# Kernel optimization log

Measured on AMD Instinct MI355X. Metric: run time of the kernel, lower is better.

## Reference

```python
import jax, jax.numpy as jnp
import numpy as np

N_HEAD = 16

def setup_inputs() -> dict:
    key = jax.random.key(0)
    ks = jax.random.split(key, 5)
    B, T, D = 2, 2048, 1024
    BN = 1024  # bottleneck_dim
    s = 0.02
    return {
        "x": jax.random.normal(ks[0], (B, T, D), dtype=jnp.float32),
        "w_qkv": jax.random.normal(ks[1], (3 * BN, D), dtype=jnp.float32) * s,
        "b_qkv": jax.random.normal(ks[2], (3 * BN,), dtype=jnp.float32) * s,
        "w_proj": jax.random.normal(ks[3], (D, BN), dtype=jnp.float32) * s,
        "b_proj": jax.random.normal(ks[4], (D,), dtype=jnp.float32) * s,
        "top_k": 64,
    }

def reference(x, w_qkv, b_qkv, w_proj, b_proj, top_k):
    B, T, D = x.shape
    H = N_HEAD
    BN = w_qkv.shape[0] // 3
    Dh = BN // H
    # qkv projection; torch Linear: y = x @ W^T + b
    qkv = (x @ w_qkv.T + b_qkv).reshape(B, T, 3, H, Dh)
    q = jnp.moveaxis(qkv[:, :, 0], 1, 2)  # (B,H,T,Dh)
    k = jnp.moveaxis(qkv[:, :, 1], 1, 2)
    v = jnp.moveaxis(qkv[:, :, 2], 1, 2)
    att = jnp.einsum('bhqd,bhkd->bhqk', q, k) * (1.0 / np.sqrt(Dh).astype(np.float32))
    # SparseK mask: keep only top-k scores per query row, mask rest before softmax
    topv = jax.lax.top_k(att, top_k)[0]          # (B,H,T,top_k)
    thresh = topv[..., -1:]                      # kth largest per row
    att = jnp.where(att >= thresh, att, -jnp.inf)
    att = jax.nn.softmax(att, axis=-1)
    y = jnp.einsum('bhqk,bhkd->bhqd', att, v)    # (B,H,T,Dh)
    y = y.transpose(0, 2, 1, 3).reshape(B, T, BN)
    return y @ w_proj.T + b_proj
```

## Files before the change

### kernel.cpp

```cpp
#include <hip/hip_runtime.h>
#include <hip/hip_bf16.h>
#include <math.h>

#define Bz 2
#define Tz 2048
#define Dz 1024
#define Hz 16
#define DHz 64
#define BNz 1024
#define TOPKz 64
#define QBLK 16
#define CAND_MAX 176
#define BAND 8e-5f
#define SLO  -20.0f
#define SBINW 0.15625f
#define SBINR 6.4f
#define LDSB 40
#define HSTR 257

typedef __attribute__((ext_vector_type(8))) short bf16x8;
typedef __attribute__((ext_vector_type(4))) short s16x4;
typedef __attribute__((ext_vector_type(4))) float f32x4;

__device__ __forceinline__ short f2bf(float f) {
  unsigned u = __float_as_uint(f);
  return (short)((u + 0x7FFFu + ((u >> 16) & 1u)) >> 16);
}
__device__ __forceinline__ float bf2f(short b) {
  return __uint_as_float(((unsigned)(unsigned short)b) << 16);
}
__device__ __forceinline__ unsigned f2s(float f) {
  unsigned u = __float_as_uint(f);
  return (u & 0x80000000u) ? ~u : (u | 0x80000000u);
}
__device__ __forceinline__ float s2f(unsigned u) {
  return __uint_as_float((u & 0x80000000u) ? (u & 0x7FFFFFFFu) : ~u);
}

__global__ __launch_bounds__(256) void qkv_gemm_split(
    const float* __restrict__ A, const float* __restrict__ W,
    const float* __restrict__ bias,
    float* __restrict__ q32, float* __restrict__ k32,
    short* __restrict__ kbf, float* __restrict__ v32)
{
  __shared__ __align__(16) short Ah[128][LDSB];
  __shared__ __align__(16) short Am[128][LDSB];
  __shared__ __align__(16) short Al[128][LDSB];
  __shared__ __align__(16) short Bh[64][LDSB];
  __shared__ __align__(16) short Bm[64][LDSB];
  __shared__ __align__(16) short Bl[64][LDSB];

  const int tid = threadIdx.x;
  const int lane = tid & 63, wid = tid >> 6;
  const int m0 = blockIdx.y * 128, n0 = blockIdx.x * 64;
  const int bcol = lane & 15, lgrp = lane >> 4;

  f32x4 acch[2][4], accl[2][4];
#pragma unroll
  for (int ms = 0; ms < 2; ++ms)
#pragma unroll
    for (int nt = 0; nt < 4; ++nt) {
      acch[ms][nt] = (f32x4){0.f, 0.f, 0.f, 0.f};
      accl[ms][nt] = (f32x4){0.f, 0.f, 0.f, 0.f};
    }

  const int arow = tid >> 1, ak = (tid & 1) * 16;
  const int brow = tid >> 2, bk = (tid & 3) * 8;
  const float* Ald = A + (size_t)(m0 + arow) * Dz + ak;
  const float* Wld = W + (size_t)(n0 + brow) * Dz + bk;

  for (int kt = 0; kt < Dz; kt += 32) {
    float4 a4[4], b4[2];
#pragma unroll
    for (int j = 0; j < 4; ++j) a4[j] = *(const float4*)(Ald + kt + 4*j);
#pragma unroll
    for (int j = 0; j < 2; ++j) b4[j] = *(const float4*)(Wld + kt + 4*j);
    __syncthreads();

#pragma unroll
    for (int j = 0; j < 4; ++j) {
      float vv[4] = {a4[j].x, a4[j].y, a4[j].z, a4[j].w};
      s16x4 h4, m4, l4;
#pragma unroll
      for (int e = 0; e < 4; ++e) {
        short hh = f2bf(vv[e]);
        float r1 = vv[e] - bf2f(hh);
        short mm = f2bf(r1);
        float r2 = r1 - bf2f(mm);
        h4[e] = hh; m4[e] = mm; l4[e] = f2bf(r2);
      }
      *(s16x4*)&Ah[arow][ak + 4*j] = h4;
      *(s16x4*)&Am[arow][ak + 4*j] = m4;
      *(s16x4*)&Al[arow][ak + 4*j] = l4;
    }
#pragma unroll
    for (int j = 0; j < 2; ++j) {
      float vv[4] = {b4[j].x, b4[j].y, b4[j].z, b4[j].w};
      s16x4 h4, m4, l4;
#pragma unroll
      for (int e = 0; e < 4; ++e) {
        short hh = f2bf(vv[e]);
        float r1 = vv[e] - bf2f(hh);
        short mm = f2bf(r1);
        float r2 = r1 - bf2f(mm);
        h4[e] = hh; m4[e] = mm; l4[e] = f2bf(r2);
      }
      *(s16x4*)&Bh[brow][bk + 4*j] = h4;
      *(s16x4*)&Bm[brow][bk + 4*j] = m4;
      *(s16x4*)&Bl[brow][bk + 4*j] = l4;
    }
    __syncthreads();

    bf16x8 ah[2], am[2], al[2];
#pragma unroll
    for (int ms = 0; ms < 2; ++ms) {
      int rr = wid*32 + ms*16 + bcol;
      ah[ms] = *(const bf16x8*)&Ah[rr][lgrp*8];
      am[ms] = *(const bf16x8*)&Am[rr][lgrp*8];
      al[ms] = *(const bf16x8*)&Al[rr][lgrp*8];
    }
#pragma unroll
    for (int nt = 0; nt < 4; ++nt) {
      int nr = nt*16 + bcol;
      bf16x8 bh = *(const bf16x8*)&Bh[nr][lgrp*8];
      bf16x8 bm = *(const bf16x8*)&Bm[nr][lgrp*8];
      bf16x8 bl = *(const bf16x8*)&Bl[nr][lgrp*8];
#pragma unroll
      for (int ms = 0; ms < 2; ++ms) {
        acch[ms][nt] = __builtin_amdgcn_mfma_f32_16x16x32_bf16(ah[ms], bh, acch[ms][nt], 0, 0, 0);
        accl[ms][nt] = __builtin_amdgcn_mfma_f32_16x16x32_bf16(ah[ms], bm, accl[ms][nt], 0, 0, 0);
        accl[ms][nt] = __builtin_amdgcn_mfma_f32_16x16x32_bf16(am[ms], bh, accl[ms][nt], 0, 0, 0);
        accl[ms][nt] = __builtin_amdgcn_mfma_f32_16x16x32_bf16(am[ms], bm, accl[ms][nt], 0, 0, 0);
        accl[ms][nt] = __builtin_amdgcn_mfma_f32_16x16x32_bf16(ah[ms], bl, accl[ms][nt], 0, 0, 0);
        accl[ms][nt] = __builtin_amdgcn_mfma_f32_16x16x32_bf16(al[ms], bh, accl[ms][nt], 0, 0, 0);
      }
    }
  }

#pragma unroll
  for (int ms = 0; ms < 2; ++ms)
#pragma unroll
    for (int nt = 0; nt < 4; ++nt)
#pragma unroll
      for (int rv = 0; rv < 4; ++rv) {
        int m = m0 + wid*32 + ms*16 + lgrp*4 + rv;
        int n = n0 + nt*16 + bcol;
        double val = (double)acch[ms][nt][rv] + (double)accl[ms][nt][rv] + (double)bias[n];
        int bb = m >> 11;
        int t = m & 2047;
        if (n < BNz) {
          int h = n >> 6, d = n & 63;
          q32[(((size_t)(bb*Hz + h))*Tz + t)*DHz + d] = (float)val;
        } else if (n < 2*BNz) {
          int h = (n - BNz) >> 6, d = n & 63;
          size_t bh = (size_t)(bb*Hz + h);
          float vf = (float)val;
          k32[(bh*Tz + t)*DHz + d] = vf;
          kbf[(bh*Tz + t)*DHz + d] = f2bf(vf);
        } else {
          int h = (n - 2*BNz) >> 6, d = n & 63;
          v32[(((size_t)(bb*Hz + h))*Tz + t)*DHz + d] = (float)val;
        }
      }
}

__global__ __launch_bounds__(256) void proj_gemm_split(
    const float* __restrict__ A, const float* __restrict__ W,
    const float* __restrict__ bias, float* __restrict__ out)
{
  __shared__ __align__(16) short Ah[128][LDSB];
  __shared__ __align__(16) short Am[128][LDSB];
  __shared__ __align__(16) short Al[128][LDSB];
  __shared__ __align__(16) short Bh[64][LDSB];
  __shared__ __align__(16) short Bm[64][LDSB];
  __shared__ __align__(16) short Bl[64][LDSB];

  const int tid = threadIdx.x;
  const int lane = tid & 63, wid = tid >> 6;
  const int m0 = blockIdx.y * 128, n0 = blockIdx.x * 64;
  const int bcol = lane & 15, lgrp = lane >> 4;

  f32x4 acch[2][4], accl[2][4];
#pragma unroll
  for (int ms = 0; ms < 2; ++ms)
#pragma unroll
    for (int nt = 0; nt < 4; ++nt) {
      acch[ms][nt] = (f32x4){0.f, 0.f, 0.f, 0.f};
      accl[ms][nt] = (f32x4){0.f, 0.f, 0.f, 0.f};
    }

  const int arow = tid >> 1, ak = (tid & 1) * 16;
  const int brow = tid >> 2, bk = (tid & 3) * 8;
  const float* Ald = A + (size_t)(m0 + arow) * Dz + ak;
  const float* Wld = W + (size_t)(n0 + brow) * Dz + bk;

  for (int kt = 0; kt < Dz; kt += 32) {
    float4 a4[4], b4[2];
#pragma unroll
    for (int j = 0; j < 4; ++j) a4[j] = *(const float4*)(Ald + kt + 4*j);
#pragma unroll
    for (int j = 0; j < 2; ++j) b4[j] = *(const float4*)(Wld + kt + 4*j);
    __syncthreads();

#pragma unroll
    for (int j = 0; j < 4; ++j) {
      float vv[4] = {a4[j].x, a4[j].y, a4[j].z, a4[j].w};
      s16x4 h4, m4, l4;
#pragma unroll
      for (int e = 0; e < 4; ++e) {
        short hh = f2bf(vv[e]);
        float r1 = vv[e] - bf2f(hh);
        short mm = f2bf(r1);
        float r2 = r1 - bf2f(mm);
        h4[e] = hh; m4[e] = mm; l4[e] = f2bf(r2);
      }
      *(s16x4*)&Ah[arow][ak + 4*j] = h4;
      *(s16x4*)&Am[arow][ak + 4*j] = m4;
      *(s16x4*)&Al[arow][ak + 4*j] = l4;
    }
#pragma unroll
    for (int j = 0; j < 2; ++j) {
      float vv[4] = {b4[j].x, b4[j].y, b4[j].z, b4[j].w};
      s16x4 h4, m4, l4;
#pragma unroll
      for (int e = 0; e < 4; ++e) {
        short hh = f2bf(vv[e]);
        float r1 = vv[e] - bf2f(hh);
        short mm = f2bf(r1);
        float r2 = r1 - bf2f(mm);
        h4[e] = hh; m4[e] = mm; l4[e] = f2bf(r2);
      }
      *(s16x4*)&Bh[brow][bk + 4*j] = h4;
      *(s16x4*)&Bm[brow][bk + 4*j] = m4;
      *(s16x4*)&Bl[brow][bk + 4*j] = l4;
    }
    __syncthreads();

    bf16x8 ah[2], am[2], al[2];
#pragma unroll
    for (int ms = 0; ms < 2; ++ms) {
      int rr = wid*32 + ms*16 + bcol;
      ah[ms] = *(const bf16x8*)&Ah[rr][lgrp*8];
      am[ms] = *(const bf16x8*)&Am[rr][lgrp*8];
      al[ms] = *(const bf16x8*)&Al[rr][lgrp*8];
    }
#pragma unroll
    for (int nt = 0; nt < 4; ++nt) {
      int nr = nt*16 + bcol;
      bf16x8 bh = *(const bf16x8*)&Bh[nr][lgrp*8];
      bf16x8 bm = *(const bf16x8*)&Bm[nr][lgrp*8];
      bf16x8 bl = *(const bf16x8*)&Bl[nr][lgrp*8];
#pragma unroll
      for (int ms = 0; ms < 2; ++ms) {
        acch[ms][nt] = __builtin_amdgcn_mfma_f32_16x16x32_bf16(ah[ms], bh, acch[ms][nt], 0, 0, 0);
        accl[ms][nt] = __builtin_amdgcn_mfma_f32_16x16x32_bf16(ah[ms], bm, accl[ms][nt], 0, 0, 0);
        accl[ms][nt] = __builtin_amdgcn_mfma_f32_16x16x32_bf16(am[ms], bh, accl[ms][nt], 0, 0, 0);
        accl[ms][nt] = __builtin_amdgcn_mfma_f32_16x16x32_bf16(am[ms], bm, accl[ms][nt], 0, 0, 0);
        accl[ms][nt] = __builtin_amdgcn_mfma_f32_16x16x32_bf16(ah[ms], bl, accl[ms][nt], 0, 0, 0);
        accl[ms][nt] = __builtin_amdgcn_mfma_f32_16x16x32_bf16(al[ms], bh, accl[ms][nt], 0, 0, 0);
      }
    }
  }

#pragma unroll
  for (int ms = 0; ms < 2; ++ms)
#pragma unroll
    for (int nt = 0; nt < 4; ++nt)
#pragma unroll
      for (int rv = 0; rv < 4; ++rv) {
        int m = m0 + wid*32 + ms*16 + lgrp*4 + rv;
        int n = n0 + nt*16 + bcol;
        out[(size_t)m * Dz + n] = (acch[ms][nt][rv] + accl[ms][nt][rv]) + bias[n];
      }
}

__global__ __launch_bounds__(256) void attn_topk(
    const float* __restrict__ q32g, const float* __restrict__ k32g,
    const short* __restrict__ kbfg, const float* __restrict__ v32,
    float* __restrict__ y)
{
  __shared__ float q_s[QBLK][DHz];
  __shared__ __align__(16) unsigned char ubuf[QBLK*CAND_MAX*6];
  __shared__ int bstar_s[QBLK];
  __shared__ int candcnt[QBLK];

  unsigned* hist = (unsigned*)ubuf;
  float* candv = (float*)ubuf;
  unsigned short* candidx = (unsigned short*)(ubuf + QBLK*CAND_MAX*4);

  const int tid = threadIdx.x;
  const int bid0 = blockIdx.x;
  const int bh_f = (bid0 & 7) + 8 * (bid0 >> 10);
  const int qbf = (bid0 >> 3) & 127;
  const int h = bh_f & 15;
  const int bb = bh_f >> 4;
  const size_t bh = (size_t)(bb * Hz + h);
  const float* qg = q32g + (bh * Tz + (size_t)qbf * QBLK) * DHz;
  const float* kg32 = k32g + bh * Tz * DHz;
  const short* kb = kbfg + bh * Tz * DHz;
  const float* vg = v32 + bh * Tz * DHz;

  if (tid < QBLK) candcnt[tid] = 0;
  for (int i = tid; i < QBLK*HSTR; i += 256) hist[i] = 0u;
  {
    int r = tid >> 4, d4 = (tid & 15) * 4;
    *(float4*)&q_s[r][d4] = *(const float4*)&qg[r*DHz + d4];
  }
  __syncthreads();

  const int lane = tid & 63;
  const int wid = tid >> 6;
  const int bcol = lane & 15;
  const int lgrp = lane >> 4;
  bf16x8 aF0, aF1;
#pragma unroll
  for (int e = 0; e < 8; ++e) {
    aF0[e] = f2bf(q_s[bcol][lgrp*8 + e]);
    aF1[e] = f2bf(q_s[bcol][32 + lgrp*8 + e]);
  }
  const int t0base = wid * 512;

  unsigned binreg[32];
#pragma unroll 4
  for (int tt = 0; tt < 32; ++tt) {
    const short* kbp = kb + (size_t)(t0base + tt*16 + bcol) * DHz;
    bf16x8 b0 = *(const bf16x8*)(kbp + lgrp*8);
    bf16x8 b1 = *(const bf16x8*)(kbp + 32 + lgrp*8);
    f32x4 c = {0.f, 0.f, 0.f, 0.f};
    c = __builtin_amdgcn_mfma_f32_16x16x32_bf16(aF0, b0, c, 0, 0, 0);
    c = __builtin_amdgcn_mfma_f32_16x16x32_bf16(aF1, b1, c, 0, 0, 0);
    unsigned bw = 0u;
#pragma unroll
    for (int j = 0; j < 4; ++j) {
      int bin = (int)((c[j] - SLO) * SBINR);
      bin = bin < 0 ? 0 : (bin > 255 ? 255 : bin);
      atomicAdd(&hist[(lgrp*4 + j)*HSTR + bin], 1u);
      bw |= ((unsigned)bin) << (8*j);
    }
    binreg[tt] = bw;
  }
  __syncthreads();

  {
    int r = tid >> 4, i16 = tid & 15;
    int s = 0;
#pragma unroll
    for (int j = 0; j < 16; ++j) s += (int)hist[r*HSTR + i16*16 + j];
    int S = s;
#pragma unroll
    for (int off = 1; off < 16; off <<= 1) {
      int src = i16 + off;
      int v = __shfl(S, (lane & 48) | (src < 16 ? src : 15));
      S += (src < 16) ? v : 0;
    }
    unsigned long long blt = __ballot(S >= TOPKz);
    unsigned mask16 = (unsigned)((blt >> (lane & 48)) & 0xFFFFull);
    int istar = 31 - __builtin_clz(mask16);
    if (i16 == istar) {
      int cum = S - s;
      int b = istar * 16;
      for (int j = 15; j >= 0; --j) {
        cum += (int)hist[r*HSTR + istar*16 + j];
        if (cum >= TOPKz) { b = istar*16 + j; break; }
      }
      bstar_s[r] = b;
    }
  }
  __syncthreads();

  {
    int bc[4];
#pragma unroll
    for (int j = 0; j < 4; ++j) {
      int b = bstar_s[lgrp*4 + j] - 1;
      bc[j] = b < 0 ? 0 : b;
    }
#pragma unroll
    for (int tt = 0; tt < 32; ++tt) {
      unsigned bw = binreg[tt];
#pragma unroll
      for (int j = 0; j < 4; ++j) {
        int bin = (int)((bw >> (8*j)) & 255u);
        if (bin >= bc[j]) {
          int r = lgrp*4 + j;
          int p = atomicAdd(&candcnt[r], 1);
          if (p < CAND_MAX) candidx[r*CAND_MAX + p] = (unsigned short)(t0base + tt*16 + bcol);
        }
      }
    }
  }
  __syncthreads();

  {
    const int r = tid >> 4, i16 = tid & 15;
    int n = candcnt[r]; if (n > CAND_MAX) n = CAND_MAX;

    for (int i = i16; i < n; i += 16) {
      int col = (int)candidx[r*CAND_MAX + i];
      const float* kpd = kg32 + (size_t)col * DHz;
      double s = 0.0;
#pragma unroll
      for (int d = 0; d < DHz; d += 4) {
        float4 k4 = *(const float4*)(kpd + d);
        s = fma((double)q_s[r][d+0], (double)k4.x, s);
        s = fma((double)q_s[r][d+1], (double)k4.y, s);
        s = fma((double)q_s[r][d+2], (double)k4.z, s);
        s = fma((double)q_s[r][d+3], (double)k4.w, s);
      }
      candv[r*CAND_MAX + i] = (float)s;
    }

    float myv[11];
    float mx = -3.0e38f;
#pragma unroll
    for (int j = 0; j < 11; ++j) {
      int i = i16 + j*16;
      float x = (i < n) ? candv[r*CAND_MAX + i] : -3.0e38f;
      myv[j] = x;
      mx = fmaxf(mx, x);
    }
#pragma unroll
    for (int m = 1; m < 16; m <<= 1) mx = fmaxf(mx, __shfl_xor(mx, m));

    float mn = 3.0e38f;
#pragma unroll
    for (int j = 0; j < 11; ++j) {
      int i = i16 + j*16;
      if (i < n) mn = fminf(mn, myv[j]);
    }
#pragma unroll
    for (int m = 1; m < 16; m <<= 1) mn = fminf(mn, __shfl_xor(mn, m));
    unsigned lo_u = f2s(mn);
    unsigned hi_u = f2s(mx) + 1u;
    while (hi_u - lo_u > 1u) {
      unsigned mid = lo_u + ((hi_u - lo_u) >> 1);
      float tv = s2f(mid);
      int cnt = 0;
#pragma unroll
      for (int j = 0; j < 11; ++j) cnt += (myv[j] >= tv) ? 1 : 0;
#pragma unroll
      for (int m = 1; m < 16; m <<= 1) cnt += __shfl_xor(cnt, m);
      if (cnt >= TOPKz) lo_u = mid; else hi_u = mid;
    }
    const float T = s2f(lo_u);

    int na = 0, nb = 0;
#pragma unroll
    for (int j = 0; j < 11; ++j) {
      float s = myv[j];
      if (s > T + BAND) na++;
      else if (s >= T - BAND) nb++;
    }
#pragma unroll
    for (int m = 1; m < 16; m <<= 1) {
      na += __shfl_xor(na, m);
      nb += __shfl_xor(nb, m);
    }
    const float wb = (float)(TOPKz - na) / (float)(nb > 0 ? nb : 1);

    float lsum = 0.f;
#pragma unroll
    for (int j = 0; j < 11; ++j) {
      int i = i16 + j*16;
      if (i < n) {
        float s = myv[j];
        float w = (s > T + BAND) ? 1.f : ((s >= T - BAND) ? wb : 0.f);
        float p = (w > 0.f) ? w * expf((s - mx) * 0.125f) : 0.f;
        candv[r*CAND_MAX + i] = p;
        lsum += p;
      }
    }
#pragma unroll
    for (int m = 1; m < 16; m <<= 1) lsum += __shfl_xor(lsum, m);
    const float rd = 1.0f / lsum;

    const int dg = i16 * 4;
    float4 o = make_float4(0.f, 0.f, 0.f, 0.f);
    for (int i = 0; i < n; ++i) {
      float p = candv[r*CAND_MAX + i];
      int idx = (int)candidx[r*CAND_MAX + i];
      float4 vv = *(const float4*)&vg[(size_t)idx*DHz + dg];
      float pw = p * rd;
      o.x = fmaf(pw, vv.x, o.x);
      o.y = fmaf(pw, vv.y, o.y);
      o.z = fmaf(pw, vv.z, o.z);
      o.w = fmaf(pw, vv.w, o.w);
    }
    float* yo = y + ((size_t)bb*Tz + (size_t)qbf*QBLK + r) * BNz + h*DHz + dg;
    *(float4*)yo = o;
  }
}

extern "C" void kernel_launch(void* const* d_in, const int* in_sizes, int n_in,
                              void* d_out, int out_size, void* d_ws, size_t ws_size,
                              hipStream_t stream)
{
  const float* x      = (const float*)d_in[0];
  const float* w_qkv  = (const float*)d_in[1];
  const float* b_qkv  = (const float*)d_in[2];
  const float* w_proj = (const float*)d_in[3];
  const float* b_proj = (const float*)d_in[4];
  float* out = (float*)d_out;

  const size_t E = (size_t)Bz * Hz * Tz * DHz;
  float* q32  = (float*)d_ws;
  float* k32  = q32 + E;
  short* kbf  = (short*)(k32 + E);
  float* v32  = (float*)(kbf + E);
  float* y    = v32 + E;

  qkv_gemm_split<<<dim3((3*BNz)/64, (Bz*Tz)/128), 256, 0, stream>>>(x, w_qkv, b_qkv, q32, k32, kbf, v32);
  attn_topk<<<Bz*Hz*(Tz/QBLK), 256, 0, stream>>>(q32, k32, kbf, v32, y);
  proj_gemm_split<<<dim3(Dz/64, (Bz*Tz)/128), 256, 0, stream>>>(y, w_proj, b_proj, out);
}
```

Baseline: 633.3 us.

## Precompute bf16 three-way splits in separate kernels before GEMMs

Moves the fp32-to-bf16 hi/mid/lo splitting of activations and weights out of the GEMM inner loops into standalone elementwise split kernels that write three bf16 planes to workspace. The GEMMs then load the preconverted bf16 planes and copy them straight into LDS, so each tile is no longer reconverted redundantly across the many blocks that read it. In exchange it adds four extra launches, extra global traffic (three bf16 planes read instead of one fp32 array), and a larger workspace.

```diff
diff --git a/kernel.cpp b/kernel.cpp
--- a/kernel.cpp
+++ b/kernel.cpp
@@ -37,8 +37,32 @@
   return __uint_as_float((u & 0x80000000u) ? (u & 0x7FFFFFFFu) : ~u);
 }
 
-__global__ __launch_bounds__(256) void qkv_gemm_split(
-    const float* __restrict__ A, const float* __restrict__ W,
+__global__ __launch_bounds__(256) void split3(
+    const float* __restrict__ in, short* __restrict__ hh,
+    short* __restrict__ mm, short* __restrict__ ll, int n4)
+{
+  int i = blockIdx.x * 256 + threadIdx.x;
+  if (i >= n4) return;
+  float4 v = ((const float4*)in)[i];
+  float vv[4] = {v.x, v.y, v.z, v.w};
+  s16x4 h4, m4, l4;
+#pragma unroll
+  for (int e = 0; e < 4; ++e) {
+    short h = f2bf(vv[e]);
+    float r1 = vv[e] - bf2f(h);
+    short m = f2bf(r1);
+    float r2 = r1 - bf2f(m);
+    h4[e] = h; m4[e] = m; l4[e] = f2bf(r2);
+  }
+  ((s16x4*)hh)[i] = h4;
+  ((s16x4*)mm)[i] = m4;
+  ((s16x4*)ll)[i] = l4;
+}
+
+__global__ __launch_bounds__(256) void qkv_gemm_v2(
+    const short* __restrict__ Axh, const short* __restrict__ Axm,
+    const short* __restrict__ Axl, const short* __restrict__ Bwh,
+    const short* __restrict__ Bwm, const short* __restrict__ Bwl,
     const float* __restrict__ bias,
     float* __restrict__ q32, float* __restrict__ k32,
     short* __restrict__ kbf, float* __restrict__ v32)
@@ -66,58 +90,35 @@
 
   const int arow = tid >> 1, ak = (tid & 1) * 16;
   const int brow = tid >> 2, bk = (tid & 3) * 8;
-  const float* Ald = A + (size_t)(m0 + arow) * Dz + ak;
-  const float* Wld = W + (size_t)(n0 + brow) * Dz + bk;
+  const size_t aoff = (size_t)(m0 + arow) * Dz + ak;
+  const size_t boff = (size_t)(n0 + brow) * Dz + bk;
 
   for (int kt = 0; kt < Dz; kt += 32) {
-    float4 a4[4], b4[2];
-#pragma unroll
-    for (int j = 0; j < 4; ++j) a4[j] = *(const float4*)(Ald + kt + 4*j);
-#pragma unroll
-    for (int j = 0; j < 2; ++j) b4[j] = *(const float4*)(Wld + kt + 4*j);
+    bf16x8 ah0 = *(const bf16x8*)(Axh + aoff + kt);
+    bf16x8 ah1 = *(const bf16x8*)(Axh + aoff + kt + 8);
+    bf16x8 am0 = *(const bf16x8*)(Axm + aoff + kt);
+    bf16x8 am1 = *(const bf16x8*)(Axm + aoff + kt + 8);
+    bf16x8 al0 = *(const bf16x8*)(Axl + aoff + kt);
+    bf16x8 al1 = *(const bf16x8*)(Axl + aoff + kt + 8);
+    bf16x8 bh8 = *(const bf16x8*)(Bwh + boff + kt);
+    bf16x8 bm8 = *(const bf16x8*)(Bwm + boff + kt);
+    bf16x8 bl8 = *(const bf16x8*)(Bwl + boff + kt);
     __syncthreads();
-
-#pragma unroll
-    for (int j = 0; j < 4; ++j) {
-      float vv[4] = {a4[j].x, a4[j].y, a4[j].z, a4[j].w};
-      s16x4 h4, m4, l4;
-#pragma unroll
-      for (int e = 0; e < 4; ++e) {
-        short hh = f2bf(vv[e]);
-        float r1 = vv[e] - bf2f(hh);
-        short mm = f2bf(r1);
-        float r2 = r1 - bf2f(mm);
-        h4[e] = hh; m4[e] = mm; l4[e] = f2bf(r2);
-      }
-      *(s16x4*)&Ah[arow][ak + 4*j] = h4;
-      *(s16x4*)&Am[arow][ak + 4*j] = m4;
-      *(s16x4*)&Al[arow][ak + 4*j] = l4;
-    }
-#pragma unroll
-    for (int j = 0; j < 2; ++j) {
-      float vv[4] = {b4[j].x, b4[j].y, b4[j].z, b4[j].w};
-      s16x4 h4, m4, l4;
-#pragma unroll
-      for (int e = 0; e < 4; ++e) {
-        short hh = f2bf(vv[e]);
-        float r1 = vv[e] - bf2f(hh);
-        short mm = f2bf(r1);
-        float r2 = r1 - bf2f(mm);
-        h4[e] = hh; m4[e] = mm; l4[e] = f2bf(r2);
-      }
-      *(s16x4*)&Bh[brow][bk + 4*j] = h4;
-      *(s16x4*)&Bm[brow][bk + 4*j] = m4;
-      *(s16x4*)&Bl[brow][bk + 4*j] = l4;
-    }
+    *(bf16x8*)&Ah[arow][ak] = ah0;  *(bf16x8*)&Ah[arow][ak+8] = ah1;
+    *(bf16x8*)&Am[arow][ak] = am0;  *(bf16x8*)&Am[arow][ak+8] = am1;
+    *(bf16x8*)&Al[arow][ak] = al0;  *(bf16x8*)&Al[arow][ak+8] = al1;
+    *(bf16x8*)&Bh[brow][bk] = bh8;
+    *(bf16x8*)&Bm[brow][bk] = bm8;
+    *(bf16x8*)&Bl[brow][bk] = bl8;
     __syncthreads();
 
-    bf16x8 ah[2], am[2], al[2];
+    bf16x8 ahf[2], amf[2], alf[2];
 #pragma unroll
     for (int ms = 0; ms < 2; ++ms) {
       int rr = wid*32 + ms*16 + bcol;
-      ah[ms] = *(const bf16x8*)&Ah[rr][lgrp*8];
-      am[ms] = *(const bf16x8*)&Am[rr][lgrp*8];
-      al[ms] = *(const bf16x8*)&Al[rr][lgrp*8];
+      ahf[ms] = *(const bf16x8*)&Ah[rr][lgrp*8];
+      amf[ms] = *(const bf16x8*)&Am[rr][lgrp*8];
+      alf[ms] = *(const bf16x8*)&Al[rr][lgrp*8];
     }
 #pragma unroll
     for (int nt = 0; nt < 4; ++nt) {
@@ -127,12 +128,12 @@
       bf16x8 bl = *(const bf16x8*)&Bl[nr][lgrp*8];
 #pragma unroll
       for (int ms = 0; ms < 2; ++ms) {
-        acch[ms][nt] = __builtin_amdgcn_mfma_f32_16x16x32_bf16(ah[ms], bh, acch[ms][nt], 0, 0, 0);
-        accl[ms][nt] = __builtin_amdgcn_mfma_f32_16x16x32_bf16(ah[ms], bm, accl[ms][nt], 0, 0, 0);
-        accl[ms][nt] = __builtin_amdgcn_mfma_f32_16x16x32_bf16(am[ms], bh, accl[ms][nt], 0, 0, 0);
-        accl[ms][nt] = __builtin_amdgcn_mfma_f32_16x16x32_bf16(am[ms], bm, accl[ms][nt], 0, 0, 0);
-        accl[ms][nt] = __builtin_amdgcn_mfma_f32_16x16x32_bf16(ah[ms], bl, accl[ms][nt], 0, 0, 0);
-        accl[ms][nt] = __builtin_amdgcn_mfma_f32_16x16x32_bf16(al[ms], bh, accl[ms][nt], 0, 0, 0);
+        acch[ms][nt] = __builtin_amdgcn_mfma_f32_16x16x32_bf16(ahf[ms], bh, acch[ms][nt], 0, 0, 0);
+        accl[ms][nt] = __builtin_amdgcn_mfma_f32_16x16x32_bf16(ahf[ms], bm, accl[ms][nt], 0, 0, 0);
+        accl[ms][nt] = __builtin_amdgcn_mfma_f32_16x16x32_bf16(amf[ms], bh, accl[ms][nt], 0, 0, 0);
+        accl[ms][nt] = __builtin_amdgcn_mfma_f32_16x16x32_bf16(amf[ms], bm, accl[ms][nt], 0, 0, 0);
+        accl[ms][nt] = __builtin_amdgcn_mfma_f32_16x16x32_bf16(ahf[ms], bl, accl[ms][nt], 0, 0, 0);
+        accl[ms][nt] = __builtin_amdgcn_mfma_f32_16x16x32_bf16(alf[ms], bh, accl[ms][nt], 0, 0, 0);
       }
     }
   }
@@ -164,8 +165,10 @@
       }
 }
 
-__global__ __launch_bounds__(256) void proj_gemm_split(
-    const float* __restrict__ A, const float* __restrict__ W,
+__global__ __launch_bounds__(256) void proj_gemm_v2(
+    const short* __restrict__ Ayh, const short* __restrict__ Aym,
+    const short* __restrict__ Ayl, const short* __restrict__ Bwh,
+    const short* __restrict__ Bwm, const short* __restrict__ Bwl,
     const float* __restrict__ bias, float* __restrict__ out)
 {
   __shared__ __align__(16) short Ah[128][LDSB];
@@ -191,58 +194,35 @@
 
   const int arow = tid >> 1, ak = (tid & 1) * 16;
   const int brow = tid >> 2, bk = (tid & 3) * 8;
-  const float* Ald = A + (size_t)(m0 + arow) * Dz + ak;
-  const float* Wld = W + (size_t)(n0 + brow) * Dz + bk;
+  const size_t aoff = (size_t)(m0 + arow) * Dz + ak;
+  const size_t boff = (size_t)(n0 + brow) * Dz + bk;
 
   for (int kt = 0; kt < Dz; kt += 32) {
-    float4 a4[4], b4[2];
-#pragma unroll
-    for (int j = 0; j < 4; ++j) a4[j] = *(const float4*)(Ald + kt + 4*j);
-#pragma unroll
-    for (int j = 0; j < 2; ++j) b4[j] = *(const float4*)(Wld + kt + 4*j);
+    bf16x8 ah0 = *(const bf16x8*)(Ayh + aoff + kt);
+    bf16x8 ah1 = *(const bf16x8*)(Ayh + aoff + kt + 8);
+    bf16x8 am0 = *(const bf16x8*)(Aym + aoff + kt);
+    bf16x8 am1 = *(const bf16x8*)(Aym + aoff + kt + 8);
+    bf16x8 al0 = *(const bf16x8*)(Ayl + aoff + kt);
+    bf16x8 al1 = *(const bf16x8*)(Ayl + aoff + kt + 8);
+    bf16x8 bh8 = *(const bf16x8*)(Bwh + boff + kt);
+    bf16x8 bm8 = *(const bf16x8*)(Bwm + boff + kt);
+    bf16x8 bl8 = *(const bf16x8*)(Bwl + boff + kt);
     __syncthreads();
-
-#pragma unroll
-    for (int j = 0; j < 4; ++j) {
-      float vv[4] = {a4[j].x, a4[j].y, a4[j].z, a4[j].w};
-      s16x4 h4, m4, l4;
-#pragma unroll
-      for (int e = 0; e < 4; ++e) {
-        short hh = f2bf(vv[e]);
-        float r1 = vv[e] - bf2f(hh);
-        short mm = f2bf(r1);
-        float r2 = r1 - bf2f(mm);
-        h4[e] = hh; m4[e] = mm; l4[e] = f2bf(r2);
-      }
-      *(s16x4*)&Ah[arow][ak + 4*j] = h4;
-      *(s16x4*)&Am[arow][ak + 4*j] = m4;
-      *(s16x4*)&Al[arow][ak + 4*j] = l4;
-    }
-#pragma unroll
-    for (int j = 0; j < 2; ++j) {
-      float vv[4] = {b4[j].x, b4[j].y, b4[j].z, b4[j].w};
-      s16x4 h4, m4, l4;
-#pragma unroll
-      for (int e = 0; e < 4; ++e) {
-        short hh = f2bf(vv[e]);
-        float r1 = vv[e] - bf2f(hh);
-        short mm = f2bf(r1);
-        float r2 = r1 - bf2f(mm);
-        h4[e] = hh; m4[e] = mm; l4[e] = f2bf(r2);
-      }
-      *(s16x4*)&Bh[brow][bk + 4*j] = h4;
-      *(s16x4*)&Bm[brow][bk + 4*j] = m4;
-      *(s16x4*)&Bl[brow][bk + 4*j] = l4;
-    }
+    *(bf16x8*)&Ah[arow][ak] = ah0;  *(bf16x8*)&Ah[arow][ak+8] = ah1;
+    *(bf16x8*)&Am[arow][ak] = am0;  *(bf16x8*)&Am[arow][ak+8] = am1;
+    *(bf16x8*)&Al[arow][ak] = al0;  *(bf16x8*)&Al[arow][ak+8] = al1;
+    *(bf16x8*)&Bh[brow][bk] = bh8;
+    *(bf16x8*)&Bm[brow][bk] = bm8;
+    *(bf16x8*)&Bl[brow][bk] = bl8;
     __syncthreads();
 
-    bf16x8 ah[2], am[2], al[2];
+    bf16x8 ahf[2], amf[2], alf[2];
 #pragma unroll
     for (int ms = 0; ms < 2; ++ms) {
       int rr = wid*32 + ms*16 + bcol;
-      ah[ms] = *(const bf16x8*)&Ah[rr][lgrp*8];
-      am[ms] = *(const bf16x8*)&Am[rr][lgrp*8];
-      al[ms] = *(const bf16x8*)&Al[rr][lgrp*8];
+      ahf[ms] = *(const bf16x8*)&Ah[rr][lgrp*8];
+      amf[ms] = *(const bf16x8*)&Am[rr][lgrp*8];
+      alf[ms] = *(const bf16x8*)&Al[rr][lgrp*8];
     }
 #pragma unroll
     for (int nt = 0; nt < 4; ++nt) {
@@ -252,12 +232,12 @@
       bf16x8 bl = *(const bf16x8*)&Bl[nr][lgrp*8];
 #pragma unroll
       for (int ms = 0; ms < 2; ++ms) {
-        acch[ms][nt] = __builtin_amdgcn_mfma_f32_16x16x32_bf16(ah[ms], bh, acch[ms][nt], 0, 0, 0);
-        accl[ms][nt] = __builtin_amdgcn_mfma_f32_16x16x32_bf16(ah[ms], bm, accl[ms][nt], 0, 0, 0);
-        accl[ms][nt] = __builtin_amdgcn_mfma_f32_16x16x32_bf16(am[ms], bh, accl[ms][nt], 0, 0, 0);
-        accl[ms][nt] = __builtin_amdgcn_mfma_f32_16x16x32_bf16(am[ms], bm, accl[ms][nt], 0, 0, 0);
-        accl[ms][nt] = __builtin_amdgcn_mfma_f32_16x16x32_bf16(ah[ms], bl, accl[ms][nt], 0, 0, 0);
-        accl[ms][nt] = __builtin_amdgcn_mfma_f32_16x16x32_bf16(al[ms], bh, accl[ms][nt], 0, 0, 0);
+        acch[ms][nt] = __builtin_amdgcn_mfma_f32_16x16x32_bf16(ahf[ms], bh, acch[ms][nt], 0, 0, 0);
+        accl[ms][nt] = __builtin_amdgcn_mfma_f32_16x16x32_bf16(ahf[ms], bm, accl[ms][nt], 0, 0, 0);
+        accl[ms][nt] = __builtin_amdgcn_mfma_f32_16x16x32_bf16(amf[ms], bh, accl[ms][nt], 0, 0, 0);
+        accl[ms][nt] = __builtin_amdgcn_mfma_f32_16x16x32_bf16(amf[ms], bm, accl[ms][nt], 0, 0, 0);
+        accl[ms][nt] = __builtin_amdgcn_mfma_f32_16x16x32_bf16(ahf[ms], bl, accl[ms][nt], 0, 0, 0);
+        accl[ms][nt] = __builtin_amdgcn_mfma_f32_16x16x32_bf16(alf[ms], bh, accl[ms][nt], 0, 0, 0);
       }
     }
   }
@@ -502,14 +482,29 @@
   const float* b_proj = (const float*)d_in[4];
   float* out = (float*)d_out;
 
-  const size_t E = (size_t)Bz * Hz * Tz * DHz;
-  float* q32  = (float*)d_ws;
-  float* k32  = q32 + E;
-  short* kbf  = (short*)(k32 + E);
-  float* v32  = (float*)(kbf + E);
-  float* y    = v32 + E;
-
-  qkv_gemm_split<<<dim3((3*BNz)/64, (Bz*Tz)/128), 256, 0, stream>>>(x, w_qkv, b_qkv, q32, k32, kbf, v32);
+  const size_t E  = (size_t)Bz * Tz * Dz;
+  const size_t Wq = (size_t)3 * BNz * Dz;
+  const size_t Wp = (size_t)Dz * BNz;
+
+  float* q32 = (float*)d_ws;
+  float* k32 = q32 + E;
+  short* kbf = (short*)(k32 + E);
+  float* v32 = (float*)(kbf + E);
+  float* y   = v32 + E;
+  short* sAh = (short*)(y + E);
+  short* sAm = sAh + E;
+  short* sAl = sAm + E;
+  short* sBh = sAl + E;
+  short* sBm = sBh + Wq;
+  short* sBl = sBm + Wq;
+
+  split3<<<(int)(E/4/256), 256, 0, stream>>>(x, sAh, sAm, sAl, (int)(E/4));
+  split3<<<(int)(Wq/4/256), 256, 0, stream>>>(w_qkv, sBh, sBm, sBl, (int)(Wq/4));
+  qkv_gemm_v2<<<dim3((3*BNz)/64, (Bz*Tz)/128), 256, 0, stream>>>(
+      sAh, sAm, sAl, sBh, sBm, sBl, b_qkv, q32, k32, kbf, v32);
   attn_topk<<<Bz*Hz*(Tz/QBLK), 256, 0, stream>>>(q32, k32, kbf, v32, y);
-  proj_gemm_split<<<dim3(Dz/64, (Bz*Tz)/128), 256, 0, stream>>>(y, w_proj, b_proj, out);
-}
+  split3<<<(int)(E/4/256), 256, 0, stream>>>(y, sAh, sAm, sAl, (int)(E/4));
+  split3<<<(int)(Wp/4/256), 256, 0, stream>>>(w_proj, sBh, sBm, sBl, (int)(Wp/4));
+  proj_gemm_v2<<<dim3(Dz/64, (Bz*Tz)/128), 256, 0, stream>>>(
+      sAh, sAm, sAl, sBh, sBm, sBl, b_proj, out);
+}
```

Measured after the change: 601.8 us (median of 2 runs). -5.0%, faster.
